# Kernel tuning notes

Hardware: AMD Instinct MI355X
Metric: run time of the kernel (lower is better)

Reference implementation:

```python
import jax, jax.numpy as jnp
import numpy as np

B, N, IN_DIM, DIM, HEADS = 2, 4096, 1024, 1024, 8
MAX_MASK = 2048
SCALE = DIM ** -0.5  # original uses full dim, not per-head dim


def setup_inputs() -> dict:
    key = jax.random.key(0)
    k_x, k_qkv, k_o, k_b, k_m = jax.random.split(key, 5)
    x = jax.random.normal(k_x, (B, N, IN_DIM), dtype=jnp.float32)
    W_qkv = jax.random.normal(k_qkv, (IN_DIM, 3 * DIM), dtype=jnp.float32) * 0.02
    W_out = jax.random.normal(k_o, (DIM, DIM), dtype=jnp.float32) * 0.02
    b_out = jax.random.normal(k_b, (DIM,), dtype=jnp.float32) * 0.02
    mask = jax.random.randint(k_m, (1, 1, MAX_MASK, MAX_MASK), 0, 2, dtype=jnp.int32)
    return {"x": x, "W_qkv": W_qkv, "W_out": W_out, "b_out": b_out,
            "mask": mask, "max_mask": MAX_MASK}


def reference(x, W_qkv, W_out, b_out, mask, max_mask):
    b, n, _ = x.shape
    d = DIM // HEADS
    qkv = x @ W_qkv                                   # [b, n, 3*dim]
    qkv = qkv.reshape(b, n, 3, HEADS, d).transpose(2, 0, 3, 1, 4)  # [3, b, h, n, d]
    q, k, v = qkv[0], qkv[1], qkv[2]
    dots = jnp.einsum('bhid,bhjd->bhij', q, k) * SCALE  # [b, h, n, n]
    # partial submatrix masking on the top-left [max_mask, max_mask] block
    m = max_mask
    sub = jnp.where(mask == 0, -jnp.inf, dots[:, :, :m, :m])
    dots = dots.at[:, :, :m, :m].set(sub)
    attn = jax.nn.softmax(dots, axis=-1)
    out = jnp.einsum('bhij,bhjd->bhid', attn, v)       # [b, h, n, d]
    out = out.transpose(0, 2, 1, 3).reshape(b, n, HEADS * d)
    return out @ W_out + b_out
```

## Files before the change

### kernel.cpp

```cpp
#include <hip/hip_runtime.h>
#include <hip/hip_bf16.h>
#include <stdint.h>


typedef __attribute__((ext_vector_type(8))) short short8;
typedef __attribute__((ext_vector_type(4))) float f32x4;

#define SCALE_Q 0.0450842200f

__device__ __forceinline__ unsigned short f2bf(float f) {
  union { float f; unsigned int u; } v;
  v.f = f;
  return (unsigned short)((v.u + 0x7fffu + ((v.u >> 16) & 1u)) >> 16);
}

__device__ __forceinline__ unsigned int pkbf2(float a, float b) {
  __hip_bfloat162 h = __float22bfloat162_rn(make_float2(a, b));
  union { __hip_bfloat162 h; unsigned int u; } c;
  c.h = h;
  return c.u;
}

__device__ __forceinline__ void gload_lds16(const void* g, void* l) {
  __builtin_amdgcn_global_load_lds(
      (const __attribute__((address_space(1))) uint32_t*)(uintptr_t)g,
      (__attribute__((address_space(3))) uint32_t*)(uintptr_t)l, 16, 0, 0);
}

__device__ __forceinline__ f32x4 zero4() {
  f32x4 z; z.x = 0.f; z.y = 0.f; z.z = 0.f; z.w = 0.f; return z;
}

__global__ __launch_bounds__(256) void k_cvt_x(const float* __restrict__ in,
                                               unsigned short* __restrict__ out) {
  const int t = blockIdx.x * 256 + threadIdx.x;
  const float4 v = ((const float4*)in)[t];
  ushort4 o;
  o.x = f2bf(v.x); o.y = f2bf(v.y); o.z = f2bf(v.z); o.w = f2bf(v.w);
  ((ushort4*)out)[t] = o;
}

__global__ __launch_bounds__(256) void k_cvt_wt(const float* __restrict__ w,
                                                unsigned short* __restrict__ wt,
                                                int Nn) {
  __shared__ float t[32][33];
  const int n0 = blockIdx.x << 5, k0 = blockIdx.y << 5;
  const int c = threadIdx.x & 31, r8 = threadIdx.x >> 5;
#pragma unroll
  for (int i = 0; i < 4; ++i) {
    const int r = (i << 3) + r8;
    t[r][c] = w[(long)(k0 + r) * Nn + n0 + c];
  }
  __syncthreads();
#pragma unroll
  for (int i = 0; i < 4; ++i) {
    const int r = (i << 3) + r8;
    wt[(long)(n0 + r) * 1024 + k0 + c] = f2bf(t[c][r]);
  }
}

__global__ __launch_bounds__(256) void k_mask_bits(
    const int* __restrict__ m, unsigned long long* __restrict__ mb) {
  const int t = blockIdx.x * 256 + threadIdx.x;
  const unsigned long long b = __ballot(m[t] != 0);
  if ((threadIdx.x & 63) == 0) mb[t >> 6] = b;
}

__global__ __launch_bounds__(256, 2) void k_qkv_gemm(
    const unsigned short* __restrict__ A,
    const unsigned short* __restrict__ Bt,
    unsigned short* __restrict__ Qs, unsigned short* __restrict__ Ks,
    unsigned short* __restrict__ Vt) {
  __shared__ __align__(16) unsigned short lA[4][128][8];
  __shared__ __align__(16) unsigned short lB[4][128][8];
  const int tid = threadIdx.x;
  const int w = tid >> 6, ln = tid & 63;
  const int m15 = ln & 15, q4 = ln >> 4;
  const int wm = (w >> 1) << 6, wn = (w & 1) << 6;
  const int id = blockIdx.x;
  const int swz = (id & 7) * 192 + (id >> 3);
  const int tn = swz % 24, tm = swz / 24;
  const int which = tn >> 3;
  const int h = tn & 7;

  f32x4 acc[4][4];
#pragma unroll
  for (int i = 0; i < 4; ++i)
#pragma unroll
    for (int j = 0; j < 4; ++j) acc[i][j] = zero4();

  if (which == 2) {
    for (int kb = 0; kb < 1024; kb += 32) {
      __syncthreads();
#pragma unroll
      for (int c = 0; c < 2; ++c) {
        const int p = ((c * 4 + w) << 10) + (ln << 4);
        const int g = p >> 11;
        const int r = (p & 2047) >> 4;
        gload_lds16(A + ((long)tm * 128 + r) * 1024 + kb + g * 8,
                    (char*)&lA[0][0][0] + p);
        gload_lds16(Bt + ((long)tn * 128 + r) * 1024 + kb + g * 8,
                    (char*)&lB[0][0][0] + p);
      }
      __syncthreads();
      short8 afr[4], bfr[4];
#pragma unroll
      for (int i = 0; i < 4; ++i)
        afr[i] = *(const short8*)&lA[q4][wm + i * 16 + m15][0];
#pragma unroll
      for (int j = 0; j < 4; ++j)
        bfr[j] = *(const short8*)&lB[q4][wn + j * 16 + m15][0];
#pragma unroll
      for (int i = 0; i < 4; ++i)
#pragma unroll
        for (int j = 0; j < 4; ++j)
          acc[i][j] = __builtin_amdgcn_mfma_f32_16x16x32_bf16(afr[i], bfr[j],
                                                              acc[i][j], 0, 0, 0);
    }
#pragma unroll
    for (int i = 0; i < 4; ++i) {
      const int m0 = (tm << 7) + wm + (i << 4) + (q4 << 2);
      const int b = m0 >> 12, row0 = m0 & 4095;
#pragma unroll
      for (int j = 0; j < 4; ++j) {
        const int dd = wn + (j << 4) + m15;
        const long bh = b * 8 + h;
        uint2 u;
        u.x = pkbf2(acc[i][j][0], acc[i][j][1]);
        u.y = pkbf2(acc[i][j][2], acc[i][j][3]);
        *(uint2*)&Vt[(bh * 128 + dd) * 4096 + row0] = u;
      }
    }
  } else {
    for (int kb = 0; kb < 1024; kb += 32) {
      __syncthreads();
#pragma unroll
      for (int c = 0; c < 2; ++c) {
        const int p = ((c * 4 + w) << 10) + (ln << 4);
        const int g = p >> 11;
        const int r = (p & 2047) >> 4;
        gload_lds16(A + ((long)tm * 128 + r) * 1024 + kb + g * 8,
                    (char*)&lA[0][0][0] + p);
        gload_lds16(Bt + ((long)tn * 128 + r) * 1024 + kb + g * 8,
                    (char*)&lB[0][0][0] + p);
      }
      __syncthreads();
      short8 afr[4], bfr[4];
#pragma unroll
      for (int i = 0; i < 4; ++i)
        afr[i] = *(const short8*)&lA[q4][wm + i * 16 + m15][0];
#pragma unroll
      for (int j = 0; j < 4; ++j)
        bfr[j] = *(const short8*)&lB[q4][wn + j * 16 + m15][0];
#pragma unroll
      for (int i = 0; i < 4; ++i)
#pragma unroll
        for (int j = 0; j < 4; ++j)
          acc[i][j] = __builtin_amdgcn_mfma_f32_16x16x32_bf16(bfr[j], afr[i],
                                                              acc[i][j], 0, 0, 0);
    }
    unsigned short* Dst = (which == 0) ? Qs : Ks;
    const float sc = (which == 0) ? SCALE_Q : 1.0f;
#pragma unroll
    for (int i = 0; i < 4; ++i) {
      const int m = (tm << 7) + wm + (i << 4) + m15;
      const int b = m >> 12, row = m & 4095;
      const long bh = b * 8 + h;
#pragma unroll
      for (int j = 0; j < 4; ++j) {
        const int dd0 = wn + (j << 4) + (q4 << 2);
        uint2 u;
        u.x = pkbf2(acc[i][j][0] * sc, acc[i][j][1] * sc);
        u.y = pkbf2(acc[i][j][2] * sc, acc[i][j][3] * sc);
        *(uint2*)&Dst[(bh * 4096 + row) * 128 + dd0] = u;
      }
    }
  }
}

__global__ __launch_bounds__(256, 1) void k_flash(
    const unsigned short* __restrict__ Qs, const unsigned short* __restrict__ Ks,
    const unsigned short* __restrict__ Vt,
    const unsigned long long* __restrict__ mbits,
    unsigned short* __restrict__ Ob) {
  __shared__ __align__(16) unsigned short lK[2][16][64][8];
  __shared__ __align__(16) unsigned short lV[2][8][128][8];
  __shared__ __align__(16) unsigned short lP[4][4][16][72];

  const int tid = threadIdx.x;
  const int w = tid >> 6, ln = tid & 63;
  const int m15 = ln & 15, q4 = ln >> 4;
  const int id = blockIdx.x;
  const int xcd = id & 7, jj = id >> 3;
  const int bh = (xcd << 1) | (jj >> 4);
  const int rowblk = jj & 15;
  const int rbase = rowblk * 256 + w * 64;

  const unsigned short* Qbh = Qs + (long)bh * 524288;
  const unsigned short* Kbh = Ks + (long)bh * 524288;
  const unsigned short* Vbh = Vt + (long)bh * 524288;

  short8 qf[4][4];
#pragma unroll
  for (int qg = 0; qg < 4; ++qg)
#pragma unroll
    for (int kk = 0; kk < 4; ++kk)
      qf[qg][kk] = *(const short8*)(Qbh + (long)(rbase + qg * 16 + m15) * 128 +
                                    kk * 32 + q4 * 8);

  f32x4 o[4][8];
#pragma unroll
  for (int qg = 0; qg < 4; ++qg)
#pragma unroll
    for (int j = 0; j < 8; ++j) o[qg][j] = zero4();
  f32x4 lacc[4];
#pragma unroll
  for (int qg = 0; qg < 4; ++qg) lacc[qg] = zero4();

  const bool maskblk = rowblk < 8;

#define STAGE_KV(dst, kvoff)                                              \
  {                                                                       \
    _Pragma("unroll")                                                     \
    for (int c = 0; c < 4; ++c) {                                         \
      const int p = ((c * 4 + w) << 10) + (ln << 4);                      \
      const int cs = p >> 10;                                             \
      const int j = (p & 1023) >> 4;                                      \
      gload_lds16(Kbh + (long)((kvoff) + j) * 128 + cs * 8,               \
                  (char*)&lK[dst][0][0][0] + p);                          \
    }                                                                     \
    _Pragma("unroll")                                                     \
    for (int c = 0; c < 4; ++c) {                                         \
      const int p = ((c * 4 + w) << 10) + (ln << 4);                      \
      const int cv = p >> 11;                                             \
      const int dv = (p & 2047) >> 4;                                     \
      gload_lds16(Vbh + (long)dv * 4096 + (kvoff) + cv * 8,               \
                  (char*)&lV[dst][0][0][0] + p);                          \
    }                                                                     \
  }

  STAGE_KV(0, 0);
  __syncthreads();

  int cur = 0;
  for (int kv = 0; kv < 4096; kv += 64) {
    unsigned long long mw[4];
    const bool domask = maskblk && (kv < 2048);
    if (domask) {
#pragma unroll
      for (int qg = 0; qg < 4; ++qg)
        mw[qg] = mbits[(long)(rbase + qg * 16 + m15) * 32 + (kv >> 6)];
    }

    const int nb = cur ^ 1;
    if (kv + 64 < 4096) STAGE_KV(nb, kv + 64);

    f32x4 s[4][4];
#pragma unroll
    for (int qg = 0; qg < 4; ++qg)
#pragma unroll
      for (int jt = 0; jt < 4; ++jt) s[qg][jt] = zero4();
    __builtin_amdgcn_s_setprio(1);
#pragma unroll
    for (int jt = 0; jt < 4; ++jt) {
#pragma unroll
      for (int kk = 0; kk < 4; ++kk) {
        const short8 kfr = *(const short8*)&lK[cur][kk * 4 + q4][jt * 16 + m15][0];
#pragma unroll
        for (int qg = 0; qg < 4; ++qg)
          s[qg][jt] = __builtin_amdgcn_mfma_f32_16x16x32_bf16(kfr, qf[qg][kk],
                                                              s[qg][jt], 0, 0, 0);
      }
    }
    __builtin_amdgcn_s_setprio(0);

    if (domask) {
#pragma unroll
      for (int qg = 0; qg < 4; ++qg) {
#pragma unroll
        for (int jt = 0; jt < 4; ++jt) {
          const unsigned int u =
              (jt & 2) ? (unsigned int)(mw[qg] >> 32) : (unsigned int)mw[qg];
          const int base = ((jt & 1) << 4) + (q4 << 2);
#pragma unroll
          for (int r = 0; r < 4; ++r) {
            if (!((u >> (base + r)) & 1u)) s[qg][jt][r] = -1e30f;
          }
        }
      }
    }

#pragma unroll
    for (int qg = 0; qg < 4; ++qg) {
#pragma unroll
      for (int jt = 0; jt < 4; ++jt) {
        f32x4 p;
        p.x = __builtin_amdgcn_exp2f(s[qg][jt].x);
        p.y = __builtin_amdgcn_exp2f(s[qg][jt].y);
        p.z = __builtin_amdgcn_exp2f(s[qg][jt].z);
        p.w = __builtin_amdgcn_exp2f(s[qg][jt].w);
        lacc[qg] += p;
        uint2 u;
        u.x = pkbf2(p.x, p.y);
        u.y = pkbf2(p.z, p.w);
        *(uint2*)&lP[w][qg][m15][jt * 16 + q4 * 4] = u;
      }
    }
    __asm__ volatile("s_waitcnt lgkmcnt(0)" ::: "memory");
    __builtin_amdgcn_sched_barrier(0);

    __builtin_amdgcn_s_setprio(1);
#pragma unroll
    for (int kk2 = 0; kk2 < 2; ++kk2) {
      short8 pf[4];
#pragma unroll
      for (int qg = 0; qg < 4; ++qg)
        pf[qg] = *(const short8*)&lP[w][qg][m15][kk2 * 32 + q4 * 8];
#pragma unroll
      for (int jt2 = 0; jt2 < 8; ++jt2) {
        const short8 vf = *(const short8*)&lV[cur][kk2 * 4 + q4][jt2 * 16 + m15][0];
#pragma unroll
        for (int qg = 0; qg < 4; ++qg)
          o[qg][jt2] = __builtin_amdgcn_mfma_f32_16x16x32_bf16(pf[qg], vf,
                                                               o[qg][jt2], 0, 0, 0);
      }
    }
    __builtin_amdgcn_s_setprio(0);

    __syncthreads();
    cur = nb;
  }
#undef STAGE_KV

  const int b = bh >> 3, h = bh & 7;
#pragma unroll
  for (int qg = 0; qg < 4; ++qg) {
    float lh = lacc[qg].x + lacc[qg].y + lacc[qg].z + lacc[qg].w;
    lh += __shfl_xor(lh, 16);
    lh += __shfl_xor(lh, 32);
    const float linv = 1.0f / lh;
#pragma unroll
    for (int r = 0; r < 4; ++r) {
      const float li = __shfl(linv, q4 * 4 + r);
      const int row = rbase + qg * 16 + q4 * 4 + r;
      unsigned short* op = Ob + ((long)(b * 4096 + row)) * 1024 + h * 128;
#pragma unroll
      for (int jt2 = 0; jt2 < 8; ++jt2)
        op[jt2 * 16 + m15] = f2bf(o[qg][jt2][r] * li);
    }
  }
}

__global__ __launch_bounds__(256, 2) void k_proj_gemm(
    const unsigned short* __restrict__ A,
    const unsigned short* __restrict__ Bt,
    const float* __restrict__ bias, float* __restrict__ Out) {
  __shared__ __align__(16) unsigned short lA[4][128][8];
  __shared__ __align__(16) unsigned short lB[4][128][8];
  const int tid = threadIdx.x;
  const int w = tid >> 6, ln = tid & 63;
  const int m15 = ln & 15, q4 = ln >> 4;
  const int wm = (w >> 1) << 6, wn = (w & 1) << 6;
  const int id = blockIdx.x;
  const int swz = (id & 7) * 64 + (id >> 3);
  const int tn = swz & 7, tm = swz >> 3;

  f32x4 acc[4][4];
#pragma unroll
  for (int i = 0; i < 4; ++i)
#pragma unroll
    for (int j = 0; j < 4; ++j) acc[i][j] = zero4();

  for (int kb = 0; kb < 1024; kb += 32) {
    __syncthreads();
#pragma unroll
    for (int c = 0; c < 2; ++c) {
      const int p = ((c * 4 + w) << 10) + (ln << 4);
      const int g = p >> 11;
      const int r = (p & 2047) >> 4;
      gload_lds16(A + ((long)tm * 128 + r) * 1024 + kb + g * 8,
                  (char*)&lA[0][0][0] + p);
      gload_lds16(Bt + ((long)tn * 128 + r) * 1024 + kb + g * 8,
                  (char*)&lB[0][0][0] + p);
    }
    __syncthreads();
    short8 afr[4], bfr[4];
#pragma unroll
    for (int i = 0; i < 4; ++i)
      afr[i] = *(const short8*)&lA[q4][wm + i * 16 + m15][0];
#pragma unroll
    for (int j = 0; j < 4; ++j)
      bfr[j] = *(const short8*)&lB[q4][wn + j * 16 + m15][0];
#pragma unroll
    for (int i = 0; i < 4; ++i)
#pragma unroll
      for (int j = 0; j < 4; ++j)
        acc[i][j] = __builtin_amdgcn_mfma_f32_16x16x32_bf16(afr[i], bfr[j],
                                                            acc[i][j], 0, 0, 0);
  }

#pragma unroll
  for (int i = 0; i < 4; ++i)
#pragma unroll
    for (int r = 0; r < 4; ++r) {
      const int m = (tm << 7) + wm + (i << 4) + (q4 << 2) + r;
#pragma unroll
      for (int j = 0; j < 4; ++j) {
        const int n = (tn << 7) + wn + (j << 4) + m15;
        Out[(long)m * 1024 + n] = acc[i][j][r] + bias[n];
      }
    }
}

extern "C" void kernel_launch(void* const* d_in, const int* in_sizes, int n_in,
                              void* d_out, int out_size, void* d_ws,
                              size_t ws_size, hipStream_t stream) {
  const float* x = (const float*)d_in[0];
  const float* Wqkv = (const float*)d_in[1];
  const float* Wout = (const float*)d_in[2];
  const float* bout = (const float*)d_in[3];
  const int* mask = (const int*)d_in[4];
  float* out = (float*)d_out;

  char* ws = (char*)d_ws;
  unsigned short* xb     = (unsigned short*)(ws);
  unsigned short* wqkv_t = (unsigned short*)(ws + 16777216);
  unsigned short* wout_t = (unsigned short*)(ws + 23068672);
  unsigned short* Qs     = (unsigned short*)(ws + 25165824);
  unsigned short* Ks     = (unsigned short*)(ws + 41943040);
  unsigned short* Vt     = (unsigned short*)(ws + 58720256);
  unsigned short* Ob     = xb;
  unsigned long long* mbits = (unsigned long long*)wqkv_t;

  hipLaunchKernelGGL(k_cvt_x, dim3(8192), dim3(256), 0, stream, x, xb);
  hipLaunchKernelGGL(k_cvt_wt, dim3(96, 32), dim3(256), 0, stream, Wqkv, wqkv_t, 3072);
  hipLaunchKernelGGL(k_cvt_wt, dim3(32, 32), dim3(256), 0, stream, Wout, wout_t, 1024);
  hipLaunchKernelGGL(k_qkv_gemm, dim3(1536), dim3(256), 0, stream,
                     xb, wqkv_t, Qs, Ks, Vt);
  hipLaunchKernelGGL(k_mask_bits, dim3(16384), dim3(256), 0, stream,
                     mask, mbits);
  hipLaunchKernelGGL(k_flash, dim3(256), dim3(256), 0, stream,
                     Qs, Ks, Vt, mbits, Ob);
  hipLaunchKernelGGL(k_proj_gemm, dim3(512), dim3(256), 0, stream,
                     Ob, wout_t, bout, out);
}
```

Before: 484.1 us.

## Rework flash attention to 32x32 MFMA with register-resident P and smaller tiles

The flash-attention kernel switches from 16x16x32 to 32x32x16 bf16 MFMA tiles. Each wave now owns 32 query rows instead of 64, and the block count doubles to 512 with two blocks per CU. The softmax probabilities are repacked in registers with cross-half lane shuffles and fed straight into the PV MFMA, which removes the LDS round trip for P and its lgkmcnt wait. Smaller per-wave tiles cut register pressure so two blocks can be resident, at the cost of reloading K/V per 128-row block rather than per 256 rows and extra shuffle instructions.

After: 431.0 us. 11.0% less time.

```diff
diff --git a/kernel.cpp b/kernel.cpp
--- a/kernel.cpp
+++ b/kernel.cpp
@@ -5,6 +5,7 @@
 
 typedef __attribute__((ext_vector_type(8))) short short8;
 typedef __attribute__((ext_vector_type(4))) float f32x4;
+typedef __attribute__((ext_vector_type(16))) float f32x16;
 
 #define SCALE_Q 0.0450842200f
 
@@ -178,46 +179,42 @@
   }
 }
 
-__global__ __launch_bounds__(256, 1) void k_flash(
+__global__ __launch_bounds__(256, 2) void k_flash(
     const unsigned short* __restrict__ Qs, const unsigned short* __restrict__ Ks,
     const unsigned short* __restrict__ Vt,
     const unsigned long long* __restrict__ mbits,
     unsigned short* __restrict__ Ob) {
   __shared__ __align__(16) unsigned short lK[2][16][64][8];
   __shared__ __align__(16) unsigned short lV[2][8][128][8];
-  __shared__ __align__(16) unsigned short lP[4][4][16][72];
 
   const int tid = threadIdx.x;
   const int w = tid >> 6, ln = tid & 63;
-  const int m15 = ln & 15, q4 = ln >> 4;
+  const int l31 = ln & 31, hi = ln >> 5, hi4 = hi << 2;
+  const bool hib = hi != 0;
   const int id = blockIdx.x;
   const int xcd = id & 7, jj = id >> 3;
-  const int bh = (xcd << 1) | (jj >> 4);
-  const int rowblk = jj & 15;
-  const int rbase = rowblk * 256 + w * 64;
+  const int bh = (xcd << 1) | (jj >> 5);
+  const int rowblk = jj & 31;
+  const int rbase = rowblk * 128 + w * 32;
+  const int qrow = rbase + l31;
 
   const unsigned short* Qbh = Qs + (long)bh * 524288;
   const unsigned short* Kbh = Ks + (long)bh * 524288;
   const unsigned short* Vbh = Vt + (long)bh * 524288;
 
-  short8 qf[4][4];
-#pragma unroll
-  for (int qg = 0; qg < 4; ++qg)
-#pragma unroll
-    for (int kk = 0; kk < 4; ++kk)
-      qf[qg][kk] = *(const short8*)(Qbh + (long)(rbase + qg * 16 + m15) * 128 +
-                                    kk * 32 + q4 * 8);
-
-  f32x4 o[4][8];
-#pragma unroll
-  for (int qg = 0; qg < 4; ++qg)
-#pragma unroll
-    for (int j = 0; j < 8; ++j) o[qg][j] = zero4();
-  f32x4 lacc[4];
-#pragma unroll
-  for (int qg = 0; qg < 4; ++qg) lacc[qg] = zero4();
-
-  const bool maskblk = rowblk < 8;
+  short8 qf[8];
+#pragma unroll
+  for (int ks = 0; ks < 8; ++ks)
+    qf[ks] = *(const short8*)(Qbh + (long)qrow * 128 + ks * 16 + hi * 8);
+
+  f32x16 o[4];
+#pragma unroll
+  for (int d = 0; d < 4; ++d)
+#pragma unroll
+    for (int r = 0; r < 16; ++r) o[d][r] = 0.f;
+  float lacc = 0.f;
+
+  const bool maskblk = rowblk < 16;
 
 #define STAGE_KV(dst, kvoff)                                              \
   {                                                                       \
@@ -239,90 +236,88 @@
     }                                                                     \
   }
 
+#define PLSWAP(a, b)                                                      \
+  {                                                                       \
+    const unsigned pa_ = (unsigned)__shfl_xor((int)(a), 32);              \
+    const unsigned pb_ = (unsigned)__shfl_xor((int)(b), 32);              \
+    const unsigned na_ = hib ? pb_ : (a);                                 \
+    const unsigned nb_ = hib ? (b) : pa_;                                 \
+    (a) = na_; (b) = nb_;                                                 \
+  }
+
   STAGE_KV(0, 0);
   __syncthreads();
 
   int cur = 0;
   for (int kv = 0; kv < 4096; kv += 64) {
-    unsigned long long mw[4];
+    unsigned long long mw = 0ull;
     const bool domask = maskblk && (kv < 2048);
-    if (domask) {
-#pragma unroll
-      for (int qg = 0; qg < 4; ++qg)
-        mw[qg] = mbits[(long)(rbase + qg * 16 + m15) * 32 + (kv >> 6)];
-    }
+    if (domask) mw = mbits[(long)qrow * 32 + (kv >> 6)];
 
     const int nb = cur ^ 1;
     if (kv + 64 < 4096) STAGE_KV(nb, kv + 64);
 
-    f32x4 s[4][4];
-#pragma unroll
-    for (int qg = 0; qg < 4; ++qg)
-#pragma unroll
-      for (int jt = 0; jt < 4; ++jt) s[qg][jt] = zero4();
+    f32x16 s0, s1;
+#pragma unroll
+    for (int r = 0; r < 16; ++r) { s0[r] = 0.f; s1[r] = 0.f; }
     __builtin_amdgcn_s_setprio(1);
 #pragma unroll
-    for (int jt = 0; jt < 4; ++jt) {
-#pragma unroll
-      for (int kk = 0; kk < 4; ++kk) {
-        const short8 kfr = *(const short8*)&lK[cur][kk * 4 + q4][jt * 16 + m15][0];
-#pragma unroll
-        for (int qg = 0; qg < 4; ++qg)
-          s[qg][jt] = __builtin_amdgcn_mfma_f32_16x16x32_bf16(kfr, qf[qg][kk],
-                                                              s[qg][jt], 0, 0, 0);
-      }
+    for (int ks = 0; ks < 8; ++ks) {
+      const short8 kf0 = *(const short8*)&lK[cur][ks * 2 + hi][l31][0];
+      const short8 kf1 = *(const short8*)&lK[cur][ks * 2 + hi][32 + l31][0];
+      s0 = __builtin_amdgcn_mfma_f32_32x32x16_bf16(kf0, qf[ks], s0, 0, 0, 0);
+      s1 = __builtin_amdgcn_mfma_f32_32x32x16_bf16(kf1, qf[ks], s1, 0, 0, 0);
     }
     __builtin_amdgcn_s_setprio(0);
 
     if (domask) {
-#pragma unroll
-      for (int qg = 0; qg < 4; ++qg) {
-#pragma unroll
-        for (int jt = 0; jt < 4; ++jt) {
-          const unsigned int u =
-              (jt & 2) ? (unsigned int)(mw[qg] >> 32) : (unsigned int)mw[qg];
-          const int base = ((jt & 1) << 4) + (q4 << 2);
-#pragma unroll
-          for (int r = 0; r < 4; ++r) {
-            if (!((u >> (base + r)) & 1u)) s[qg][jt][r] = -1e30f;
-          }
-        }
-      }
-    }
-
-#pragma unroll
-    for (int qg = 0; qg < 4; ++qg) {
-#pragma unroll
-      for (int jt = 0; jt < 4; ++jt) {
-        f32x4 p;
-        p.x = __builtin_amdgcn_exp2f(s[qg][jt].x);
-        p.y = __builtin_amdgcn_exp2f(s[qg][jt].y);
-        p.z = __builtin_amdgcn_exp2f(s[qg][jt].z);
-        p.w = __builtin_amdgcn_exp2f(s[qg][jt].w);
-        lacc[qg] += p;
-        uint2 u;
-        u.x = pkbf2(p.x, p.y);
-        u.y = pkbf2(p.z, p.w);
-        *(uint2*)&lP[w][qg][m15][jt * 16 + q4 * 4] = u;
-      }
-    }
-    __asm__ volatile("s_waitcnt lgkmcnt(0)" ::: "memory");
-    __builtin_amdgcn_sched_barrier(0);
+      const unsigned mlo = ((unsigned)mw) >> hi4;
+      const unsigned mhi = ((unsigned)(mw >> 32)) >> hi4;
+#pragma unroll
+      for (int r = 0; r < 16; ++r) {
+        const int c = ((r >> 2) << 3) + (r & 3);
+        if (!((mlo >> c) & 1u)) s0[r] = -1e30f;
+        if (!((mhi >> c) & 1u)) s1[r] = -1e30f;
+      }
+    }
+
+    float p0[16], p1[16];
+#pragma unroll
+    for (int r = 0; r < 16; ++r) {
+      p0[r] = __builtin_amdgcn_exp2f(s0[r]);
+      p1[r] = __builtin_amdgcn_exp2f(s1[r]);
+      lacc += p0[r] + p1[r];
+    }
+
+    unsigned w00 = pkbf2(p0[0], p0[1]),   w01 = pkbf2(p0[2], p0[3]);
+    unsigned w10 = pkbf2(p0[4], p0[5]),   w11 = pkbf2(p0[6], p0[7]);
+    PLSWAP(w00, w10); PLSWAP(w01, w11);
+    unsigned w20 = pkbf2(p0[8], p0[9]),   w21 = pkbf2(p0[10], p0[11]);
+    unsigned w30 = pkbf2(p0[12], p0[13]), w31 = pkbf2(p0[14], p0[15]);
+    PLSWAP(w20, w30); PLSWAP(w21, w31);
+    unsigned x00 = pkbf2(p1[0], p1[1]),   x01 = pkbf2(p1[2], p1[3]);
+    unsigned x10 = pkbf2(p1[4], p1[5]),   x11 = pkbf2(p1[6], p1[7]);
+    PLSWAP(x00, x10); PLSWAP(x01, x11);
+    unsigned x20 = pkbf2(p1[8], p1[9]),   x21 = pkbf2(p1[10], p1[11]);
+    unsigned x30 = pkbf2(p1[12], p1[13]), x31 = pkbf2(p1[14], p1[15]);
+    PLSWAP(x20, x30); PLSWAP(x21, x31);
+
+    union { unsigned u[4]; short8 s; } pa0, pa1, pa2, pa3;
+    pa0.u[0] = w00; pa0.u[1] = w01; pa0.u[2] = w10; pa0.u[3] = w11;
+    pa1.u[0] = w20; pa1.u[1] = w21; pa1.u[2] = w30; pa1.u[3] = w31;
+    pa2.u[0] = x00; pa2.u[1] = x01; pa2.u[2] = x10; pa2.u[3] = x11;
+    pa3.u[0] = x20; pa3.u[1] = x21; pa3.u[2] = x30; pa3.u[3] = x31;
+    const short8 pa[4] = {pa0.s, pa1.s, pa2.s, pa3.s};
 
     __builtin_amdgcn_s_setprio(1);
 #pragma unroll
-    for (int kk2 = 0; kk2 < 2; ++kk2) {
-      short8 pf[4];
-#pragma unroll
-      for (int qg = 0; qg < 4; ++qg)
-        pf[qg] = *(const short8*)&lP[w][qg][m15][kk2 * 32 + q4 * 8];
-#pragma unroll
-      for (int jt2 = 0; jt2 < 8; ++jt2) {
-        const short8 vf = *(const short8*)&lV[cur][kk2 * 4 + q4][jt2 * 16 + m15][0];
-#pragma unroll
-        for (int qg = 0; qg < 4; ++qg)
-          o[qg][jt2] = __builtin_amdgcn_mfma_f32_16x16x32_bf16(pf[qg], vf,
-                                                               o[qg][jt2], 0, 0, 0);
+    for (int ksl = 0; ksl < 4; ++ksl) {
+#pragma unroll
+      for (int db = 0; db < 4; ++db) {
+        const short8 vf =
+            *(const short8*)&lV[cur][ksl * 2 + hi][db * 32 + l31][0];
+        o[db] = __builtin_amdgcn_mfma_f32_32x32x16_bf16(pa[ksl], vf,
+                                                        o[db], 0, 0, 0);
       }
     }
     __builtin_amdgcn_s_setprio(0);
@@ -331,23 +326,21 @@
     cur = nb;
   }
 #undef STAGE_KV
+#undef PLSWAP
+
+  const float lh = lacc + __shfl_xor(lacc, 32);
+  const float linv = 1.0f / lh;
 
   const int b = bh >> 3, h = bh & 7;
 #pragma unroll
-  for (int qg = 0; qg < 4; ++qg) {
-    float lh = lacc[qg].x + lacc[qg].y + lacc[qg].z + lacc[qg].w;
-    lh += __shfl_xor(lh, 16);
-    lh += __shfl_xor(lh, 32);
-    const float linv = 1.0f / lh;
-#pragma unroll
-    for (int r = 0; r < 4; ++r) {
-      const float li = __shfl(linv, q4 * 4 + r);
-      const int row = rbase + qg * 16 + q4 * 4 + r;
-      unsigned short* op = Ob + ((long)(b * 4096 + row)) * 1024 + h * 128;
-#pragma unroll
-      for (int jt2 = 0; jt2 < 8; ++jt2)
-        op[jt2 * 16 + m15] = f2bf(o[qg][jt2][r] * li);
-    }
+  for (int r = 0; r < 16; ++r) {
+    const int qr = (r & 3) + ((r >> 2) << 3) + hi4;
+    const float li = __shfl(linv, qr);
+    const int row = rbase + qr;
+    unsigned short* op = Ob + ((long)(b * 4096 + row)) * 1024 + h * 128 + l31;
+#pragma unroll
+    for (int db = 0; db < 4; ++db)
+      op[db * 32] = f2bf(o[db][r] * li);
   }
 }
 
@@ -439,7 +432,7 @@
                      xb, wqkv_t, Qs, Ks, Vt);
   hipLaunchKernelGGL(k_mask_bits, dim3(16384), dim3(256), 0, stream,
                      mask, mbits);
-  hipLaunchKernelGGL(k_flash, dim3(256), dim3(256), 0, stream,
+  hipLaunchKernelGGL(k_flash, dim3(512), dim3(256), 0, stream,
                      Qs, Ks, Vt, mbits, Ob);
   hipLaunchKernelGGL(k_proj_gemm, dim3(512), dim3(256), 0, stream,
                      Ob, wout_t, bout, out);
```
